# Kernel tuning notes

Hardware: AMD Instinct MI355X
Metric: run time of the kernel (lower is better)

Reference implementation:

```python
import jax, jax.numpy as jnp
import numpy as np

BATCH = 256
MAX_STEP = 200
NUM_Q = 1000


def setup_inputs() -> dict:
    key = jax.random.key(0)
    k1, k2 = jax.random.split(key)
    # predictions strictly inside (0, 1) for BCE
    pred = jax.random.uniform(k1, (BATCH, MAX_STEP - 1, NUM_Q), dtype=jnp.float32) * 0.98 + 0.01
    # sparse binary error-ID labels; some rows all-zero -> masked out (ragged structure)
    batch = (jax.random.uniform(k2, (BATCH, MAX_STEP, NUM_Q)) < 0.002).astype(jnp.float32)
    # guarantee every student has at least one attempted row (torch BCE on empty -> NaN)
    batch = batch.at[:, 1, 0].set(1.0)
    return {"pred": pred, "batch": batch}


def reference(pred, batch):
    # ErrorIDs path: gt = batch[student][1:], keep rows containing any 1.
    gt = batch[:, 1:, :]                              # [B, T-1, Q]
    row_mask = jnp.any(gt == 1.0, axis=-1)            # [B, T-1] ragged mask
    m = row_mask[:, :, None].astype(pred.dtype)       # [B, T-1, 1]

    # nn.BCELoss: -(y*log(p) + (1-y)*log(1-p)), logs clamped at -100, mean reduction
    log_p = jnp.maximum(jnp.log(pred), -100.0)
    log_1mp = jnp.maximum(jnp.log1p(-pred), -100.0)
    bce = -(gt * log_p + (1.0 - gt) * log_1mp)        # [B, T-1, Q]

    n_elem = row_mask.sum(axis=1).astype(pred.dtype) * gt.shape[-1]  # selected elements per student
    per_student = (bce * m).sum(axis=(1, 2)) / n_elem               # mean BCE per student
    loss = per_student.sum()                                        # summed over students

    # Original returns ragged concatenations of selected rows; we return the
    # equivalent masked full tensors plus the row mask (same information, jit-friendly).
    return (loss, pred * m, gt * m, row_mask)
```

## Files before the change

kernel.cpp:

```cpp
#include <hip/hip_runtime.h>

#define BATCHN 256
#define TSTEPS 199
#define NQ     1000
#define NROWS  (BATCHN * TSTEPS)

__global__ void zero_ws_kernel(float* __restrict__ ws) {
    int i = threadIdx.x;
    if (i < 2 * BATCHN) ws[i] = 0.0f;
}

__global__ __launch_bounds__(256) void main_kernel(
    const float* __restrict__ pred,
    const float* __restrict__ batch,
    float* __restrict__ out,
    float* __restrict__ ws)
{
    const int r = blockIdx.x;
    const int b = r / TSTEPS;
    const int t = r - b * TSTEPS;
    const int i = threadIdx.x;

    const float4* p4 = (const float4*)(pred + (size_t)r * NQ);
    const float4* g4 = (const float4*)(batch + ((size_t)b * 200 + t + 1) * NQ);

    float4 p = make_float4(0.f, 0.f, 0.f, 0.f);
    float4 g = make_float4(0.f, 0.f, 0.f, 0.f);
    if (i < 250) { p = p4[i]; g = g4[i]; }

    float s = 0.0f;
    int any = 0;
    if (i < 250) {
        float pe[4] = {p.x, p.y, p.z, p.w};
        float ge[4] = {g.x, g.y, g.z, g.w};
        #pragma unroll
        for (int k = 0; k < 4; ++k) {
            any |= (ge[k] == 1.0f);
            float lp = fmaxf(__logf(pe[k]),        -100.0f);
            float l1 = fmaxf(__logf(1.0f - pe[k]), -100.0f);
            s -= l1 + ge[k] * (lp - l1);
        }
    }

    #pragma unroll
    for (int off = 32; off > 0; off >>= 1) {
        s   += __shfl_down(s, off);
        any |= __shfl_down(any, off);
    }

    __shared__ float ssum[4];
    __shared__ int   sany[4];
    const int lane = i & 63, wid = i >> 6;
    if (lane == 0) { ssum[wid] = s; sany[wid] = any; }
    __syncthreads();

    __shared__ float bsum;
    __shared__ int   bany;
    if (i == 0) {
        bsum = ssum[0] + ssum[1] + ssum[2] + ssum[3];
        bany = sany[0] | sany[1] | sany[2] | sany[3];
    }
    __syncthreads();

    const float m = bany ? 1.0f : 0.0f;

    float* out_pred = out + 1;
    float* out_gt   = out + 1 + (size_t)NROWS * NQ;
    float* out_mask = out + 1 + 2 * (size_t)NROWS * NQ;

    if (i < 250) {
        size_t o = (size_t)r * NQ + 4 * (size_t)i;
        out_pred[o + 0] = p.x * m;
        out_pred[o + 1] = p.y * m;
        out_pred[o + 2] = p.z * m;
        out_pred[o + 3] = p.w * m;
        out_gt[o + 0] = g.x * m;
        out_gt[o + 1] = g.y * m;
        out_gt[o + 2] = g.z * m;
        out_gt[o + 3] = g.w * m;
    }
    if (i == 0) {
        out_mask[r] = m;
        if (bany) {
            atomicAdd(&ws[b], bsum);
            atomicAdd(&ws[BATCHN + b], 1.0f);
        }
    }
}

__global__ __launch_bounds__(256) void final_kernel(
    float* __restrict__ out, const float* __restrict__ ws)
{
    const int b = threadIdx.x;
    float per = ws[b] / (ws[BATCHN + b] * (float)NQ);

    #pragma unroll
    for (int off = 32; off > 0; off >>= 1) per += __shfl_down(per, off);

    __shared__ float ssum[4];
    const int lane = b & 63, wid = b >> 6;
    if (lane == 0) ssum[wid] = per;
    __syncthreads();
    if (b == 0) out[0] = ssum[0] + ssum[1] + ssum[2] + ssum[3];
}

extern "C" void kernel_launch(void* const* d_in, const int* in_sizes, int n_in,
                              void* d_out, int out_size, void* d_ws, size_t ws_size,
                              hipStream_t stream) {
    const float* pred  = (const float*)d_in[0];
    const float* batch = (const float*)d_in[1];
    float* out = (float*)d_out;
    float* ws  = (float*)d_ws;

    zero_ws_kernel<<<1, 512, 0, stream>>>(ws);
    main_kernel<<<NROWS, 256, 0, stream>>>(pred, batch, out, ws);
    final_kernel<<<1, 256, 0, stream>>>(out, ws);
}
```

Baseline: 707.2 us.

## Map one row per wavefront with ballot mask and nontemporal stores

Each 64-lane wavefront now handles one row, with four float4 loads per lane, instead of one 256-thread block per row. The row mask comes from a wave ballot, which removes the shared-memory block reduction and both __syncthreads. Output writes use nontemporal stores so they do not pollute the cache. Per-row atomics go from one per block to one per wave. Some lanes sit idle on the last chunk because 250 is not a multiple of 64, and the float stores are scalar rather than float4.

```diff
diff --git a/kernel.cpp b/kernel.cpp
--- a/kernel.cpp
+++ b/kernel.cpp
@@ -4,6 +4,8 @@
 #define TSTEPS 199
 #define NQ     1000
 #define NROWS  (BATCHN * TSTEPS)
+#define ROWS_PER_BLOCK 4
+#define NBLOCKS (NROWS / ROWS_PER_BLOCK)
 
 __global__ void zero_ws_kernel(float* __restrict__ ws) {
     int i = threadIdx.x;
@@ -16,73 +18,60 @@
     float* __restrict__ out,
     float* __restrict__ ws)
 {
-    const int r = blockIdx.x;
+    const int wid  = threadIdx.x >> 6;
+    const int lane = threadIdx.x & 63;
+    const int r = blockIdx.x * ROWS_PER_BLOCK + wid;
     const int b = r / TSTEPS;
     const int t = r - b * TSTEPS;
-    const int i = threadIdx.x;
 
     const float4* p4 = (const float4*)(pred + (size_t)r * NQ);
     const float4* g4 = (const float4*)(batch + ((size_t)b * 200 + t + 1) * NQ);
 
-    float4 p = make_float4(0.f, 0.f, 0.f, 0.f);
-    float4 g = make_float4(0.f, 0.f, 0.f, 0.f);
-    if (i < 250) { p = p4[i]; g = g4[i]; }
-
-    float s = 0.0f;
-    int any = 0;
-    if (i < 250) {
-        float pe[4] = {p.x, p.y, p.z, p.w};
-        float ge[4] = {g.x, g.y, g.z, g.w};
-        #pragma unroll
-        for (int k = 0; k < 4; ++k) {
-            any |= (ge[k] == 1.0f);
-            float lp = fmaxf(__logf(pe[k]),        -100.0f);
-            float l1 = fmaxf(__logf(1.0f - pe[k]), -100.0f);
-            s -= l1 + ge[k] * (lp - l1);
-        }
+    float4 p[4], g[4];
+    #pragma unroll
+    for (int j = 0; j < 4; ++j) {
+        const int k = lane + 64 * j;
+        if (k < 250) { g[j] = g4[k]; p[j] = p4[k]; }
+        else         { g[j] = make_float4(0.f,0.f,0.f,0.f); p[j] = make_float4(0.f,0.f,0.f,0.f); }
     }
 
+    int any = 0;
     #pragma unroll
-    for (int off = 32; off > 0; off >>= 1) {
-        s   += __shfl_down(s, off);
-        any |= __shfl_down(any, off);
-    }
-
-    __shared__ float ssum[4];
-    __shared__ int   sany[4];
-    const int lane = i & 63, wid = i >> 6;
-    if (lane == 0) { ssum[wid] = s; sany[wid] = any; }
-    __syncthreads();
-
-    __shared__ float bsum;
-    __shared__ int   bany;
-    if (i == 0) {
-        bsum = ssum[0] + ssum[1] + ssum[2] + ssum[3];
-        bany = sany[0] | sany[1] | sany[2] | sany[3];
-    }
-    __syncthreads();
-
-    const float m = bany ? 1.0f : 0.0f;
+    for (int j = 0; j < 4; ++j)
+        any |= (g[j].x == 1.0f) | (g[j].y == 1.0f) | (g[j].z == 1.0f) | (g[j].w == 1.0f);
+    const unsigned long long bm = __ballot(any);
+    const float m = bm ? 1.0f : 0.0f;
 
     float* out_pred = out + 1;
     float* out_gt   = out + 1 + (size_t)NROWS * NQ;
     float* out_mask = out + 1 + 2 * (size_t)NROWS * NQ;
 
-    if (i < 250) {
-        size_t o = (size_t)r * NQ + 4 * (size_t)i;
-        out_pred[o + 0] = p.x * m;
-        out_pred[o + 1] = p.y * m;
-        out_pred[o + 2] = p.z * m;
-        out_pred[o + 3] = p.w * m;
-        out_gt[o + 0] = g.x * m;
-        out_gt[o + 1] = g.y * m;
-        out_gt[o + 2] = g.z * m;
-        out_gt[o + 3] = g.w * m;
+    float s = 0.0f;
+    #pragma unroll
+    for (int j = 0; j < 4; ++j) {
+        const int k = lane + 64 * j;
+        if (k < 250) {
+            float pe[4] = {p[j].x, p[j].y, p[j].z, p[j].w};
+            float ge[4] = {g[j].x, g[j].y, g[j].z, g[j].w};
+            const size_t o = (size_t)r * NQ + 4 * (size_t)k;
+            #pragma unroll
+            for (int q = 0; q < 4; ++q) {
+                const float lp = fmaxf(__logf(pe[q]),        -100.0f);
+                const float l1 = fmaxf(__logf(1.0f - pe[q]), -100.0f);
+                s -= l1 + ge[q] * (lp - l1);
+                __builtin_nontemporal_store(pe[q] * m, &out_pred[o + q]);
+                __builtin_nontemporal_store(ge[q] * m, &out_gt[o + q]);
+            }
+        }
     }
-    if (i == 0) {
+
+    #pragma unroll
+    for (int off = 32; off > 0; off >>= 1) s += __shfl_down(s, off);
+
+    if (lane == 0) {
         out_mask[r] = m;
-        if (bany) {
-            atomicAdd(&ws[b], bsum);
+        if (bm) {
+            atomicAdd(&ws[b], s);
             atomicAdd(&ws[BATCHN + b], 1.0f);
         }
     }
@@ -113,6 +102,6 @@
     float* ws  = (float*)d_ws;
 
     zero_ws_kernel<<<1, 512, 0, stream>>>(ws);
-    main_kernel<<<NROWS, 256, 0, stream>>>(pred, batch, out, ws);
+    main_kernel<<<NBLOCKS, 256, 0, stream>>>(pred, batch, out, ws);
     final_kernel<<<1, 256, 0, stream>>>(out, ws);
 }
```

After: 723.6 us. +2.3%, slower.
